# Optimization experiments

Measured on AMD Instinct MI355X. Metric: run time of the kernel, lower is better.

The kernel has to match this reference:

```python
import jax, jax.numpy as jnp
import numpy as np

N = 50000
E = 600000
C = 128          # out_channels (== in_channels)
L = 3            # num_conv layers
HID = 32
NUM_CLASSES = 7


def setup_inputs() -> dict:
    key = jax.random.key(0)
    ks = jax.random.split(key, 16)
    bound = 1.0 / np.sqrt(C)
    inp = {
        "x": jax.random.normal(ks[0], (N, C), dtype=jnp.float32),
        "edge_index": jax.random.randint(ks[1], (2, E), 0, N, dtype=jnp.int32),
        "edge_weight": jax.random.uniform(ks[2], (E,), dtype=jnp.float32),
        # GatedGraphConv weight: [num_layers, C, C], uniform(-1/sqrt(C), 1/sqrt(C))
        "conv_weight": jax.random.uniform(ks[3], (L, C, C), minval=-bound, maxval=bound, dtype=jnp.float32),
        # GRUCell params (torch layout: [3C, C] for ih and hh, gate order r,z,n)
        "w_ih": jax.random.uniform(ks[4], (3 * C, C), minval=-bound, maxval=bound, dtype=jnp.float32),
        "w_hh": jax.random.uniform(ks[5], (3 * C, C), minval=-bound, maxval=bound, dtype=jnp.float32),
        "b_ih": jax.random.uniform(ks[6], (3 * C,), minval=-bound, maxval=bound, dtype=jnp.float32),
        "b_hh": jax.random.uniform(ks[7], (3 * C,), minval=-bound, maxval=bound, dtype=jnp.float32),
        # MLP: C -> 32 -> 32 -> 32 -> NUM_CLASSES, tanh between hidden layers
        "w0": jax.random.normal(ks[8], (HID, C), dtype=jnp.float32) * 0.05,
        "b0": jnp.zeros((HID,), dtype=jnp.float32),
        "w1": jax.random.normal(ks[9], (HID, HID), dtype=jnp.float32) * 0.1,
        "b1": jnp.zeros((HID,), dtype=jnp.float32),
        "w2": jax.random.normal(ks[10], (HID, HID), dtype=jnp.float32) * 0.1,
        "b2": jnp.zeros((HID,), dtype=jnp.float32),
        "w3": jax.random.normal(ks[11], (NUM_CLASSES, HID), dtype=jnp.float32) * 0.1,
        "b3": jnp.zeros((NUM_CLASSES,), dtype=jnp.float32),
    }
    return inp


def _gru_cell(m, h, w_ih, w_hh, b_ih, b_hh):
    # torch GRUCell: gates ordered (r, z, n)
    gx = m @ w_ih.T + b_ih          # [N, 3C]
    gh = h @ w_hh.T + b_hh          # [N, 3C]
    xr, xz, xn = jnp.split(gx, 3, axis=-1)
    hr, hz, hn = jnp.split(gh, 3, axis=-1)
    r = jax.nn.sigmoid(xr + hr)
    z = jax.nn.sigmoid(xz + hz)
    n = jnp.tanh(xn + r * hn)
    return (1.0 - z) * n + z * h


def reference(x, edge_index, edge_weight, conv_weight, w_ih, w_hh, b_ih, b_hh,
              w0, b0, w1, b1, w2, b2, w3, b3):
    src, dst = edge_index[0], edge_index[1]
    h = x  # in_channels == out_channels, no padding needed
    for i in range(L):
        m = h @ conv_weight[i]                          # [N, C] dense GEMM
        msgs = edge_weight[:, None] * m[src]            # gather + edge weighting [E, C]
        agg = jax.ops.segment_sum(msgs, dst, num_segments=N)  # scatter-add [N, C]
        h = _gru_cell(agg, h, w_ih, w_hh, b_ih, b_hh)
    # MLP with tanh between hidden layers, linear last
    y = jnp.tanh(h @ w0.T + b0)
    y = jnp.tanh(y @ w1.T + b1)
    y = jnp.tanh(y @ w2.T + b2)
    y = y @ w3.T + b3
    return jax.nn.log_softmax(y, axis=-1)
```

## Files before the change

### kernel.cpp

```cpp
#include <hip/hip_runtime.h>
#include <hip/hip_bf16.h>
#include <math.h>

#define NN 50000
#define NE 600000
#define CC 128
#define NL 3
#define NRG (NN / 16)
#define C_RG 4
#define G_RG 4
#define SCAN_B 196

typedef __attribute__((ext_vector_type(8))) short bf16x8;
typedef __attribute__((ext_vector_type(4))) float f32x4;
typedef unsigned short ushort_t;
typedef unsigned int uint_t;

__device__ inline ushort_t f2bf(float f) {
    __hip_bfloat16 b = __float2bfloat16(f);
    return *reinterpret_cast<ushort_t*>(&b);
}
__device__ inline float bf2f(ushort_t u) {
    return __uint_as_float(((uint_t)u) << 16);
}
__device__ inline float fsig(float x) {
    return __builtin_amdgcn_rcpf(1.f + __builtin_amdgcn_exp2f(-1.44269504f * x));
}
__device__ inline float ftanh(float x) {
    float e = __builtin_amdgcn_exp2f(2.88539008f * fabsf(x));
    float t = 1.f - 2.f * __builtin_amdgcn_rcpf(e + 1.f);
    return copysignf(t, x);
}

__global__ __launch_bounds__(256) void k_prep(const float* __restrict__ x,
                                              ushort_t* __restrict__ h_bf,
                                              const float* __restrict__ wih,
                                              const float* __restrict__ whh,
                                              const float* __restrict__ cw,
                                              const float* __restrict__ w0,
                                              const float* __restrict__ w1,
                                              const float* __restrict__ w2,
                                              const float* __restrict__ w3,
                                              ushort_t* __restrict__ wx_pk,
                                              ushort_t* __restrict__ wh_pk,
                                              ushort_t* __restrict__ cw_pk,
                                              ushort_t* __restrict__ wm_pk,
                                              int* __restrict__ degcnt) {
    int bid = blockIdx.x;
    int t = threadIdx.x;
    if (bid < 6250) {
        size_t i = (size_t)bid * 256 + t;
        float4 v = ((const float4*)x)[i];
        ushort4 u;
        u.x = f2bf(v.x); u.y = f2bf(v.y); u.z = f2bf(v.z); u.w = f2bf(v.w);
        ((ushort4*)h_bf)[i] = u;
        return;
    }
    int bb = bid - 6250;
    if (bb < 384) {
        const float* W = (bb < 192) ? wih : whh;
        ushort_t* pk = (bb < 192) ? wx_pk : wh_pk;
        int tid = ((bb < 192) ? bb : bb - 192) * 256 + t;
        int e = tid & 7;
        int l = (tid >> 3) & 63;
        int s = (tid >> 9) & 3;
        int rest = tid >> 11;
        int g = rest % 3, c0 = rest / 3;
        int row = g * 128 + c0 * 16 + (l & 15);
        int col = s * 32 + (l >> 4) * 8 + e;
        pk[tid] = f2bf(W[row * 128 + col]);
        return;
    }
    bb -= 384;
    if (bb < 192) {
        int tid = bb * 256 + t;
        int e = tid & 7;
        int l = (tid >> 3) & 63;
        int s = (tid >> 9) & 3;
        int rest = tid >> 11;
        int c0 = rest & 7, layer = rest >> 3;
        int c = c0 * 16 + (l & 15);
        int k = s * 32 + (l >> 4) * 8 + e;
        cw_pk[tid] = f2bf(cw[layer * 16384 + k * 128 + c]);
        return;
    }
    bb -= 192;
    if (bb < 26) {
        int tid = bb * 256 + t;
        if (tid >= 6656) return;
        int e = tid & 7;
        int l = (tid >> 3) & 63;
        int lr = l & 15, lg = l >> 4;
        if (tid < 4096) {
            int s = (tid >> 9) & 3;
            int c0 = tid >> 11;
            wm_pk[tid] = f2bf(w0[(c0 * 16 + lr) * 128 + s * 32 + lg * 8 + e]);
        } else if (tid < 5120) {
            int c0 = (tid - 4096) >> 9;
            wm_pk[tid] = f2bf(w1[(c0 * 16 + lr) * 32 + lg * 8 + e]);
        } else if (tid < 6144) {
            int c0 = (tid - 5120) >> 9;
            wm_pk[tid] = f2bf(w2[(c0 * 16 + lr) * 32 + lg * 8 + e]);
        } else {
            wm_pk[tid] = (lr < 7) ? f2bf(w3[lr * 32 + lg * 8 + e]) : (ushort_t)0;
        }
        return;
    }
    bb -= 26;
    {
        int i = bb * 256 + t;
        if (i < 2 * NN) degcnt[i] = 0;
    }
}

__global__ __launch_bounds__(256) void k_count(const int* __restrict__ dst,
                                               int* __restrict__ deg) {
    int c = blockIdx.x * 256 + threadIdx.x;
    if (c >= NE / 4) return;
    int4 d4 = ((const int4*)dst)[c];
    atomicAdd(&deg[d4.x], 1);
    atomicAdd(&deg[d4.y], 1);
    atomicAdd(&deg[d4.z], 1);
    atomicAdd(&deg[d4.w], 1);
}

__global__ __launch_bounds__(256) void k_scan1(const int* __restrict__ deg,
                                               int* __restrict__ off,
                                               int* __restrict__ bsum) {
    __shared__ int sm[256];
    int t = threadIdx.x, i = blockIdx.x * 256 + t;
    int v = (i < NN) ? deg[i] : 0;
    sm[t] = v;
    __syncthreads();
#pragma unroll
    for (int ofs = 1; ofs < 256; ofs <<= 1) {
        int u = (t >= ofs) ? sm[t - ofs] : 0;
        __syncthreads();
        sm[t] += u;
        __syncthreads();
    }
    if (i < NN) off[i] = sm[t] - v;
    if (t == 255) bsum[blockIdx.x] = sm[255];
}

__global__ __launch_bounds__(256) void k_scan2(const int* __restrict__ bsum,
                                               int* __restrict__ bofs,
                                               int* __restrict__ off) {
    __shared__ int sm[256];
    int t = threadIdx.x;
    int v = (t < SCAN_B) ? bsum[t] : 0;
    sm[t] = v;
    __syncthreads();
#pragma unroll
    for (int ofs = 1; ofs < 256; ofs <<= 1) {
        int u = (t >= ofs) ? sm[t - ofs] : 0;
        __syncthreads();
        sm[t] += u;
        __syncthreads();
    }
    if (t < SCAN_B) bofs[t] = sm[t] - v;
    if (t == 255) off[NN] = sm[255];
}

__global__ __launch_bounds__(256) void k_fill(const int* __restrict__ src,
                                              const int* __restrict__ dst,
                                              const float* __restrict__ ew,
                                              const int* __restrict__ off_p,
                                              const int* __restrict__ bofs,
                                              int* __restrict__ cnt,
                                              uint2* __restrict__ e_pair) {
    int e = blockIdx.x * 256 + threadIdx.x;
    if (e >= NE) return;
    int d = dst[e];
    int p = off_p[d] + bofs[d >> 8] + atomicAdd(&cnt[d], 1);
    uint2 pr;
    pr.x = (uint_t)src[e];
    pr.y = __float_as_uint(ew[e]);
    e_pair[p] = pr;
}

__global__ __launch_bounds__(256, 2) void k_conv(const ushort_t* __restrict__ h_bf,
                                                 const ushort_t* __restrict__ cw_pk,
                                                 ushort_t* __restrict__ m_bf) {
    int wid = (blockIdx.x * 256 + threadIdx.x) >> 6;
    int l = threadIdx.x & 63;
    int lr = l & 15, lg = l >> 4;
    int c0g = wid & 3;
    int chunk = wid >> 2;

    bf16x8 B[2][4];
    {
        const bf16x8* pw = (const bf16x8*)cw_pk;
#pragma unroll
        for (int p = 0; p < 2; p++)
#pragma unroll
            for (int s = 0; s < 4; s++)
                B[p][s] = pw[(size_t)(((c0g + 4 * p) * 4 + s) * 64) + l];
    }
    int c_lo = c0g * 16 + lr;

    for (int it = 0; it < C_RG; it++) {
        int rg = chunk * C_RG + it;
        if (rg >= NRG) break;
        int n0 = rg * 16;
        const short* ap = (const short*)h_bf + (size_t)(n0 + lr) * CC + lg * 8;
        bf16x8 a[4];
#pragma unroll
        for (int s = 0; s < 4; s++) a[s] = *(const bf16x8*)(ap + s * 32);
        f32x4 acc0 = {0.f,0.f,0.f,0.f}, acc1 = {0.f,0.f,0.f,0.f};
#pragma unroll
        for (int s = 0; s < 4; s++) {
            acc0 = __builtin_amdgcn_mfma_f32_16x16x32_bf16(a[s], B[0][s], acc0, 0, 0, 0);
            acc1 = __builtin_amdgcn_mfma_f32_16x16x32_bf16(a[s], B[1][s], acc1, 0, 0, 0);
        }
#pragma unroll
        for (int j = 0; j < 4; j++) {
            size_t row = (size_t)(n0 + lg * 4 + j) * CC;
            m_bf[row + c_lo] = f2bf(acc0[j]);
            m_bf[row + c_lo + 64] = f2bf(acc1[j]);
        }
    }
}

__global__ __launch_bounds__(256) void k_agg(const int* __restrict__ off_p,
                                             const int* __restrict__ bofs,
                                             const uint2* __restrict__ e_pair,
                                             const ushort_t* __restrict__ m_bf,
                                             ushort_t* __restrict__ agg_bf) {
    int node = blockIdx.x * 4 + (threadIdx.x >> 6);
    int l = threadIdx.x & 63;
    int half = l >> 5, sl = l & 31;
    if (node >= NN) return;
    int b = off_p[node] + bofs[node >> 8];
    int e = (node == NN - 1) ? off_p[NN]
                             : off_p[node + 1] + bofs[(node + 1) >> 8];
    const uint2* m2 = (const uint2*)m_bf;
    float a0 = 0.f, a1 = 0.f, a2 = 0.f, a3 = 0.f;
    int i = b;
    for (; i + 8 <= e; i += 8) {
        uint2 p0 = e_pair[i + half];
        uint2 p1 = e_pair[i + 2 + half];
        uint2 p2 = e_pair[i + 4 + half];
        uint2 p3 = e_pair[i + 6 + half];
        uint2 v0 = m2[(size_t)p0.x * 32 + sl];
        uint2 v1 = m2[(size_t)p1.x * 32 + sl];
        uint2 v2 = m2[(size_t)p2.x * 32 + sl];
        uint2 v3 = m2[(size_t)p3.x * 32 + sl];
        float w0 = __uint_as_float(p0.y), w1 = __uint_as_float(p1.y);
        float w2 = __uint_as_float(p2.y), w3 = __uint_as_float(p3.y);
        a0 += w0 * bf2f((ushort_t)(v0.x & 0xffffu)) + w1 * bf2f((ushort_t)(v1.x & 0xffffu))
            + w2 * bf2f((ushort_t)(v2.x & 0xffffu)) + w3 * bf2f((ushort_t)(v3.x & 0xffffu));
        a1 += w0 * bf2f((ushort_t)(v0.x >> 16))     + w1 * bf2f((ushort_t)(v1.x >> 16))
            + w2 * bf2f((ushort_t)(v2.x >> 16))     + w3 * bf2f((ushort_t)(v3.x >> 16));
        a2 += w0 * bf2f((ushort_t)(v0.y & 0xffffu)) + w1 * bf2f((ushort_t)(v1.y & 0xffffu))
            + w2 * bf2f((ushort_t)(v2.y & 0xffffu)) + w3 * bf2f((ushort_t)(v3.y & 0xffffu));
        a3 += w0 * bf2f((ushort_t)(v0.y >> 16))     + w1 * bf2f((ushort_t)(v1.y >> 16))
            + w2 * bf2f((ushort_t)(v2.y >> 16))     + w3 * bf2f((ushort_t)(v3.y >> 16));
    }
    for (; i + 4 <= e; i += 4) {
        uint2 p0 = e_pair[i + half];
        uint2 p1 = e_pair[i + 2 + half];
        uint2 v0 = m2[(size_t)p0.x * 32 + sl];
        uint2 v1 = m2[(size_t)p1.x * 32 + sl];
        float w0 = __uint_as_float(p0.y), w1 = __uint_as_float(p1.y);
        a0 += w0 * bf2f((ushort_t)(v0.x & 0xffffu)) + w1 * bf2f((ushort_t)(v1.x & 0xffffu));
        a1 += w0 * bf2f((ushort_t)(v0.x >> 16))     + w1 * bf2f((ushort_t)(v1.x >> 16));
        a2 += w0 * bf2f((ushort_t)(v0.y & 0xffffu)) + w1 * bf2f((ushort_t)(v1.y & 0xffffu));
        a3 += w0 * bf2f((ushort_t)(v0.y >> 16))     + w1 * bf2f((ushort_t)(v1.y >> 16));
    }
    for (; i < e; i += 2) {
        int idx = i + half;
        uint2 pr = (idx < e) ? e_pair[idx] : make_uint2(0u, 0u);
        uint2 v = m2[(size_t)pr.x * 32 + sl];
        float w = __uint_as_float(pr.y);
        a0 += w * bf2f((ushort_t)(v.x & 0xffffu));
        a1 += w * bf2f((ushort_t)(v.x >> 16));
        a2 += w * bf2f((ushort_t)(v.y & 0xffffu));
        a3 += w * bf2f((ushort_t)(v.y >> 16));
    }
    a0 += __shfl_xor(a0, 32);
    a1 += __shfl_xor(a1, 32);
    a2 += __shfl_xor(a2, 32);
    a3 += __shfl_xor(a3, 32);
    if (half == 0) {
        uint2 p;
        p.x = (uint_t)f2bf(a0) | ((uint_t)f2bf(a1) << 16);
        p.y = (uint_t)f2bf(a2) | ((uint_t)f2bf(a3) << 16);
        ((uint2*)agg_bf)[(size_t)node * 32 + sl] = p;
    }
}

__global__ __launch_bounds__(256, 2) void k_gru(const ushort_t* __restrict__ agg_bf,
                                                const ushort_t* __restrict__ hbf_in,
                                                ushort_t* __restrict__ hbf_out,
                                                const ushort_t* __restrict__ wx_pk,
                                                const ushort_t* __restrict__ wh_pk,
                                                const float* __restrict__ b_ih,
                                                const float* __restrict__ b_hh) {
    int wid = (blockIdx.x * 256 + threadIdx.x) >> 6;
    int l = threadIdx.x & 63;
    int c0 = wid & 7;
    int chunk = wid >> 3;
    int lr = l & 15, lg = l >> 4;

    bf16x8 BX[12], BH[12];
    {
        const bf16x8* px = (const bf16x8*)wx_pk + (size_t)c0 * 12 * 64 + l;
        const bf16x8* ph = (const bf16x8*)wh_pk + (size_t)c0 * 12 * 64 + l;
#pragma unroll
        for (int f = 0; f < 12; f++) { BX[f] = px[f * 64]; BH[f] = ph[f * 64]; }
    }
    int c = c0 * 16 + lr;
    float bxr = b_ih[c], bxz = b_ih[128 + c], bxn = b_ih[256 + c];
    float bhr = b_hh[c], bhz = b_hh[128 + c], bhn = b_hh[256 + c];

    for (int it = 0; it < G_RG; it++) {
        int rg = chunk * G_RG + it;
        if (rg >= NRG) break;
        int n0 = rg * 16;
        const short* ap = (const short*)agg_bf + (size_t)(n0 + lr) * CC + lg * 8;
        const short* hp = (const short*)hbf_in + (size_t)(n0 + lr) * CC + lg * 8;
        bf16x8 a[4], hf[4];
#pragma unroll
        for (int s = 0; s < 4; s++) {
            a[s] = *(const bf16x8*)(ap + s * 32);
            hf[s] = *(const bf16x8*)(hp + s * 32);
        }
        float hv[4];
#pragma unroll
        for (int j = 0; j < 4; j++)
            hv[j] = bf2f(hbf_in[(size_t)(n0 + lg * 4 + j) * CC + c]);

        f32x4 r0 = {0.f,0.f,0.f,0.f}, r1 = {0.f,0.f,0.f,0.f}, r2 = {0.f,0.f,0.f,0.f};
        f32x4 r3 = {0.f,0.f,0.f,0.f}, r4 = {0.f,0.f,0.f,0.f}, r5 = {0.f,0.f,0.f,0.f};
#pragma unroll
        for (int s = 0; s < 4; s++) {
            r0 = __builtin_amdgcn_mfma_f32_16x16x32_bf16(a[s], BX[s], r0, 0, 0, 0);
            r1 = __builtin_amdgcn_mfma_f32_16x16x32_bf16(a[s], BX[4 + s], r1, 0, 0, 0);
            r2 = __builtin_amdgcn_mfma_f32_16x16x32_bf16(a[s], BX[8 + s], r2, 0, 0, 0);
            r3 = __builtin_amdgcn_mfma_f32_16x16x32_bf16(hf[s], BH[s], r3, 0, 0, 0);
            r4 = __builtin_amdgcn_mfma_f32_16x16x32_bf16(hf[s], BH[4 + s], r4, 0, 0, 0);
            r5 = __builtin_amdgcn_mfma_f32_16x16x32_bf16(hf[s], BH[8 + s], r5, 0, 0, 0);
        }
#pragma unroll
        for (int j = 0; j < 4; j++) {
            size_t row = (size_t)(n0 + lg * 4 + j);
            float rg_ = fsig(r0[j] + bxr + r3[j] + bhr);
            float zg = fsig(r1[j] + bxz + r4[j] + bhz);
            float ng = ftanh(r2[j] + bxn + rg_ * (r5[j] + bhn));
            float hn2 = (1.f - zg) * ng + zg * hv[j];
            hbf_out[row * CC + c] = f2bf(hn2);
        }
    }
}

__global__ __launch_bounds__(256, 2) void k_mlp(const ushort_t* __restrict__ hbf,
                                                const ushort_t* __restrict__ wm_pk,
                                                const float* __restrict__ b0,
                                                const float* __restrict__ b1,
                                                const float* __restrict__ b2,
                                                const float* __restrict__ b3,
                                                float* __restrict__ out) {
    __shared__ short vt[4][16][40];
    __shared__ float yt[4][16][8];
    int wid = (blockIdx.x * 256 + threadIdx.x) >> 6;
    int wq = threadIdx.x >> 6;
    int l = threadIdx.x & 63;
    int lr = l & 15, lg = l >> 4;

    bf16x8 W0[2][4], W1[2], W2[2], W3;
    {
        const bf16x8* pw = (const bf16x8*)wm_pk;
#pragma unroll
        for (int c0 = 0; c0 < 2; c0++)
#pragma unroll
            for (int s = 0; s < 4; s++) W0[c0][s] = pw[(c0 * 4 + s) * 64 + l];
#pragma unroll
        for (int c0 = 0; c0 < 2; c0++) {
            W1[c0] = pw[512 + c0 * 64 + l];
            W2[c0] = pw[640 + c0 * 64 + l];
        }
        W3 = pw[768 + l];
    }
    float b0v[2] = {b0[lr], b0[16 + lr]};
    float b1v[2] = {b1[lr], b1[16 + lr]};
    float b2v[2] = {b2[lr], b2[16 + lr]};
    float b3v = (lr < 7) ? b3[lr] : 0.f;

    if (wid >= NRG) return;
    int n0 = wid * 16;

    bf16x8 a[4];
    {
        const short* ap = (const short*)hbf + (size_t)(n0 + lr) * CC + lg * 8;
#pragma unroll
        for (int s = 0; s < 4; s++) a[s] = *(const bf16x8*)(ap + s * 32);
    }
#pragma unroll
    for (int c0 = 0; c0 < 2; c0++) {
        f32x4 acc = {0.f, 0.f, 0.f, 0.f};
#pragma unroll
        for (int s = 0; s < 4; s++)
            acc = __builtin_amdgcn_mfma_f32_16x16x32_bf16(a[s], W0[c0][s], acc, 0, 0, 0);
#pragma unroll
        for (int j = 0; j < 4; j++)
            vt[wq][lg * 4 + j][c0 * 16 + lr] = (short)f2bf(ftanh(acc[j] + b0v[c0]));
    }
    {
        bf16x8 av = *(const bf16x8*)&vt[wq][lr][lg * 8];
        f32x4 acc[2];
#pragma unroll
        for (int c0 = 0; c0 < 2; c0++) {
            f32x4 z = {0.f, 0.f, 0.f, 0.f};
            acc[c0] = __builtin_amdgcn_mfma_f32_16x16x32_bf16(av, W1[c0], z, 0, 0, 0);
        }
#pragma unroll
        for (int c0 = 0; c0 < 2; c0++)
#pragma unroll
            for (int j = 0; j < 4; j++)
                vt[wq][lg * 4 + j][c0 * 16 + lr] = (short)f2bf(ftanh(acc[c0][j] + b1v[c0]));
    }
    {
        bf16x8 av = *(const bf16x8*)&vt[wq][lr][lg * 8];
        f32x4 acc[2];
#pragma unroll
        for (int c0 = 0; c0 < 2; c0++) {
            f32x4 z = {0.f, 0.f, 0.f, 0.f};
            acc[c0] = __builtin_amdgcn_mfma_f32_16x16x32_bf16(av, W2[c0], z, 0, 0, 0);
        }
#pragma unroll
        for (int c0 = 0; c0 < 2; c0++)
#pragma unroll
            for (int j = 0; j < 4; j++)
                vt[wq][lg * 4 + j][c0 * 16 + lr] = (short)f2bf(ftanh(acc[c0][j] + b2v[c0]));
    }
    {
        bf16x8 av = *(const bf16x8*)&vt[wq][lr][lg * 8];
        f32x4 z = {0.f, 0.f, 0.f, 0.f};
        f32x4 acc = __builtin_amdgcn_mfma_f32_16x16x32_bf16(av, W3, z, 0, 0, 0);
        if (lr < 7) {
#pragma unroll
            for (int j = 0; j < 4; j++) yt[wq][lg * 4 + j][lr] = acc[j] + b3v;
        }
    }
    __builtin_amdgcn_s_waitcnt(0);
    if (l < 16) {
        float y[7];
#pragma unroll
        for (int j = 0; j < 7; j++) y[j] = yt[wq][l][j];
        float mx = y[0];
#pragma unroll
        for (int j = 1; j < 7; j++) mx = fmaxf(mx, y[j]);
        float se = 0.f;
#pragma unroll
        for (int j = 0; j < 7; j++) se += expf(y[j] - mx);
        float lse = mx + logf(se);
#pragma unroll
        for (int j = 0; j < 7; j++) out[(size_t)(n0 + l) * 7 + j] = y[j] - lse;
    }
}

extern "C" void kernel_launch(void* const* d_in, const int* in_sizes, int n_in,
                              void* d_out, int out_size, void* d_ws, size_t ws_size,
                              hipStream_t stream) {
    const float* x   = (const float*)d_in[0];
    const int*   ei  = (const int*)d_in[1];
    const float* ew  = (const float*)d_in[2];
    const float* cw  = (const float*)d_in[3];
    const float* wih = (const float*)d_in[4];
    const float* whh = (const float*)d_in[5];
    const float* bih = (const float*)d_in[6];
    const float* bhh = (const float*)d_in[7];
    const float* w0 = (const float*)d_in[8];
    const float* b0 = (const float*)d_in[9];
    const float* w1 = (const float*)d_in[10];
    const float* b1 = (const float*)d_in[11];
    const float* w2 = (const float*)d_in[12];
    const float* b2 = (const float*)d_in[13];
    const float* w3 = (const float*)d_in[14];
    const float* b3 = (const float*)d_in[15];
    float* out = (float*)d_out;

    ushort_t* hbf0  = (ushort_t*)d_ws;
    ushort_t* hbf1  = hbf0 + (size_t)NN * CC;
    ushort_t* m_bf  = hbf1 + (size_t)NN * CC;
    ushort_t* agg_bf= m_bf + (size_t)NN * CC;
    ushort_t* wx_pk = agg_bf + (size_t)NN * CC;
    ushort_t* wh_pk = wx_pk + 3 * CC * CC;
    ushort_t* cw_pk = wh_pk + 3 * CC * CC;
    ushort_t* wm_pk = cw_pk + 3 * CC * CC;
    uint2*    e_pair= (uint2*)(wm_pk + 6656);
    int*      off   = (int*)(e_pair + NE);
    int*      deg   = off + (NN + 1);
    int*      cnt   = deg + NN;
    int*      bsum  = cnt + NN;
    int*      bofs  = bsum + SCAN_B;

    const int* src = ei;
    const int* dst = ei + NE;

    k_prep<<<7243, 256, 0, stream>>>(x, hbf0, wih, whh, cw, w0, w1, w2, w3,
                                     wx_pk, wh_pk, cw_pk, wm_pk, deg);

    k_count<<<(NE / 4 + 255) / 256, 256, 0, stream>>>(dst, deg);
    k_scan1<<<SCAN_B, 256, 0, stream>>>(deg, off, bsum);
    k_scan2<<<1, 256, 0, stream>>>(bsum, bofs, off);
    k_fill<<<(NE + 255) / 256, 256, 0, stream>>>(src, dst, ew, off, bofs, cnt, e_pair);

    const int conv_waves = 4 * ((NRG + C_RG - 1) / C_RG);
    const int conv_blk = (conv_waves + 3) / 4;
    const int gru_waves = 8 * ((NRG + G_RG - 1) / G_RG);
    const int gru_blk = (gru_waves + 3) / 4;

    ushort_t* hin = hbf0;
    ushort_t* hout = hbf1;
    for (int l = 0; l < NL; l++) {
        k_conv<<<conv_blk, 256, 0, stream>>>(hin, cw_pk + (size_t)l * CC * CC, m_bf);
        k_agg<<<(NN + 3) / 4, 256, 0, stream>>>(off, bofs, e_pair, m_bf, agg_bf);
        k_gru<<<gru_blk, 256, 0, stream>>>(agg_bf, hin, hout, wx_pk, wh_pk, bih, bhh);
        ushort_t* tmp = hin; hin = hout; hout = tmp;
    }
    k_mlp<<<(NRG + 3) / 4, 256, 0, stream>>>(hin, wm_pk, b0, b1, b2, b3, out);
}
```

Before: 306.4 us.

## Fuse neighbor aggregation into GRU kernel via shared-memory staging

Merges the CSR gather/aggregate kernel and the GRU kernel into one kernel. Each 512-thread block aggregates 64 destination rows into an XOR-swizzled LDS tile, then eight waves each compute one 16-column slice of the GRU gates from that tile. This removes the global agg buffer write and read and one launch per layer. The trade-off is that each half-wave now handles a whole node's edges serially instead of splitting them across two halves, and the block waits at a barrier before the MFMA stage.

```diff
diff --git a/kernel.cpp b/kernel.cpp
--- a/kernel.cpp
+++ b/kernel.cpp
@@ -222,108 +222,97 @@
     }
 }
 
-__global__ __launch_bounds__(256) void k_agg(const int* __restrict__ off_p,
-                                             const int* __restrict__ bofs,
-                                             const uint2* __restrict__ e_pair,
-                                             const ushort_t* __restrict__ m_bf,
-                                             ushort_t* __restrict__ agg_bf) {
-    int node = blockIdx.x * 4 + (threadIdx.x >> 6);
-    int l = threadIdx.x & 63;
-    int half = l >> 5, sl = l & 31;
-    if (node >= NN) return;
-    int b = off_p[node] + bofs[node >> 8];
-    int e = (node == NN - 1) ? off_p[NN]
-                             : off_p[node + 1] + bofs[(node + 1) >> 8];
-    const uint2* m2 = (const uint2*)m_bf;
-    float a0 = 0.f, a1 = 0.f, a2 = 0.f, a3 = 0.f;
-    int i = b;
-    for (; i + 8 <= e; i += 8) {
-        uint2 p0 = e_pair[i + half];
-        uint2 p1 = e_pair[i + 2 + half];
-        uint2 p2 = e_pair[i + 4 + half];
-        uint2 p3 = e_pair[i + 6 + half];
-        uint2 v0 = m2[(size_t)p0.x * 32 + sl];
-        uint2 v1 = m2[(size_t)p1.x * 32 + sl];
-        uint2 v2 = m2[(size_t)p2.x * 32 + sl];
-        uint2 v3 = m2[(size_t)p3.x * 32 + sl];
-        float w0 = __uint_as_float(p0.y), w1 = __uint_as_float(p1.y);
-        float w2 = __uint_as_float(p2.y), w3 = __uint_as_float(p3.y);
-        a0 += w0 * bf2f((ushort_t)(v0.x & 0xffffu)) + w1 * bf2f((ushort_t)(v1.x & 0xffffu))
-            + w2 * bf2f((ushort_t)(v2.x & 0xffffu)) + w3 * bf2f((ushort_t)(v3.x & 0xffffu));
-        a1 += w0 * bf2f((ushort_t)(v0.x >> 16))     + w1 * bf2f((ushort_t)(v1.x >> 16))
-            + w2 * bf2f((ushort_t)(v2.x >> 16))     + w3 * bf2f((ushort_t)(v3.x >> 16));
-        a2 += w0 * bf2f((ushort_t)(v0.y & 0xffffu)) + w1 * bf2f((ushort_t)(v1.y & 0xffffu))
-            + w2 * bf2f((ushort_t)(v2.y & 0xffffu)) + w3 * bf2f((ushort_t)(v3.y & 0xffffu));
-        a3 += w0 * bf2f((ushort_t)(v0.y >> 16))     + w1 * bf2f((ushort_t)(v1.y >> 16))
-            + w2 * bf2f((ushort_t)(v2.y >> 16))     + w3 * bf2f((ushort_t)(v3.y >> 16));
-    }
-    for (; i + 4 <= e; i += 4) {
-        uint2 p0 = e_pair[i + half];
-        uint2 p1 = e_pair[i + 2 + half];
-        uint2 v0 = m2[(size_t)p0.x * 32 + sl];
-        uint2 v1 = m2[(size_t)p1.x * 32 + sl];
-        float w0 = __uint_as_float(p0.y), w1 = __uint_as_float(p1.y);
-        a0 += w0 * bf2f((ushort_t)(v0.x & 0xffffu)) + w1 * bf2f((ushort_t)(v1.x & 0xffffu));
-        a1 += w0 * bf2f((ushort_t)(v0.x >> 16))     + w1 * bf2f((ushort_t)(v1.x >> 16));
-        a2 += w0 * bf2f((ushort_t)(v0.y & 0xffffu)) + w1 * bf2f((ushort_t)(v1.y & 0xffffu));
-        a3 += w0 * bf2f((ushort_t)(v0.y >> 16))     + w1 * bf2f((ushort_t)(v1.y >> 16));
-    }
-    for (; i < e; i += 2) {
-        int idx = i + half;
-        uint2 pr = (idx < e) ? e_pair[idx] : make_uint2(0u, 0u);
-        uint2 v = m2[(size_t)pr.x * 32 + sl];
-        float w = __uint_as_float(pr.y);
-        a0 += w * bf2f((ushort_t)(v.x & 0xffffu));
-        a1 += w * bf2f((ushort_t)(v.x >> 16));
-        a2 += w * bf2f((ushort_t)(v.y & 0xffffu));
-        a3 += w * bf2f((ushort_t)(v.y >> 16));
-    }
-    a0 += __shfl_xor(a0, 32);
-    a1 += __shfl_xor(a1, 32);
-    a2 += __shfl_xor(a2, 32);
-    a3 += __shfl_xor(a3, 32);
-    if (half == 0) {
-        uint2 p;
-        p.x = (uint_t)f2bf(a0) | ((uint_t)f2bf(a1) << 16);
-        p.y = (uint_t)f2bf(a2) | ((uint_t)f2bf(a3) << 16);
-        ((uint2*)agg_bf)[(size_t)node * 32 + sl] = p;
-    }
-}
-
-__global__ __launch_bounds__(256, 2) void k_gru(const ushort_t* __restrict__ agg_bf,
-                                                const ushort_t* __restrict__ hbf_in,
-                                                ushort_t* __restrict__ hbf_out,
-                                                const ushort_t* __restrict__ wx_pk,
-                                                const ushort_t* __restrict__ wh_pk,
-                                                const float* __restrict__ b_ih,
-                                                const float* __restrict__ b_hh) {
-    int wid = (blockIdx.x * 256 + threadIdx.x) >> 6;
-    int l = threadIdx.x & 63;
-    int c0 = wid & 7;
-    int chunk = wid >> 3;
+__global__ __launch_bounds__(512, 2) void k_agru(const int* __restrict__ off_p,
+                                                 const int* __restrict__ bofs,
+                                                 const uint2* __restrict__ e_pair,
+                                                 const ushort_t* __restrict__ m_bf,
+                                                 const ushort_t* __restrict__ hbf_in,
+                                                 ushort_t* __restrict__ hbf_out,
+                                                 const ushort_t* __restrict__ wx_pk,
+                                                 const ushort_t* __restrict__ wh_pk,
+                                                 const float* __restrict__ b_ih,
+                                                 const float* __restrict__ b_hh) {
+    __shared__ uint_t agg_lds[64 * 64];
+    int t = threadIdx.x;
+    int w = t >> 6;
+    int l = t & 63;
     int lr = l & 15, lg = l >> 4;
+    int row0 = blockIdx.x * 64;
 
     bf16x8 BX[12], BH[12];
     {
-        const bf16x8* px = (const bf16x8*)wx_pk + (size_t)c0 * 12 * 64 + l;
-        const bf16x8* ph = (const bf16x8*)wh_pk + (size_t)c0 * 12 * 64 + l;
+        const bf16x8* px = (const bf16x8*)wx_pk + (size_t)w * 12 * 64 + l;
+        const bf16x8* ph = (const bf16x8*)wh_pk + (size_t)w * 12 * 64 + l;
 #pragma unroll
         for (int f = 0; f < 12; f++) { BX[f] = px[f * 64]; BH[f] = ph[f * 64]; }
     }
-    int c = c0 * 16 + lr;
+
+    {
+        int hw = t >> 5;
+        int sl = t & 31;
+        const uint2* m2 = (const uint2*)m_bf;
+#pragma unroll
+        for (int k = 0; k < 4; k++) {
+            int r = hw * 4 + k;
+            int node = row0 + r;
+            if (node < NN) {
+                int b = off_p[node] + bofs[node >> 8];
+                int e = (node == NN - 1) ? off_p[NN]
+                                         : off_p[node + 1] + bofs[(node + 1) >> 8];
+                float a0 = 0.f, a1 = 0.f, a2 = 0.f, a3 = 0.f;
+                int i = b;
+                for (; i + 4 <= e; i += 4) {
+                    uint2 p0 = e_pair[i], p1 = e_pair[i + 1];
+                    uint2 p2 = e_pair[i + 2], p3 = e_pair[i + 3];
+                    uint2 v0 = m2[(size_t)p0.x * 32 + sl];
+                    uint2 v1 = m2[(size_t)p1.x * 32 + sl];
+                    uint2 v2 = m2[(size_t)p2.x * 32 + sl];
+                    uint2 v3 = m2[(size_t)p3.x * 32 + sl];
+                    float w0 = __uint_as_float(p0.y), w1 = __uint_as_float(p1.y);
+                    float w2 = __uint_as_float(p2.y), w3 = __uint_as_float(p3.y);
+                    a0 += w0 * bf2f((ushort_t)(v0.x & 0xffffu)) + w1 * bf2f((ushort_t)(v1.x & 0xffffu))
+                        + w2 * bf2f((ushort_t)(v2.x & 0xffffu)) + w3 * bf2f((ushort_t)(v3.x & 0xffffu));
+                    a1 += w0 * bf2f((ushort_t)(v0.x >> 16))     + w1 * bf2f((ushort_t)(v1.x >> 16))
+                        + w2 * bf2f((ushort_t)(v2.x >> 16))     + w3 * bf2f((ushort_t)(v3.x >> 16));
+                    a2 += w0 * bf2f((ushort_t)(v0.y & 0xffffu)) + w1 * bf2f((ushort_t)(v1.y & 0xffffu))
+                        + w2 * bf2f((ushort_t)(v2.y & 0xffffu)) + w3 * bf2f((ushort_t)(v3.y & 0xffffu));
+                    a3 += w0 * bf2f((ushort_t)(v0.y >> 16))     + w1 * bf2f((ushort_t)(v1.y >> 16))
+                        + w2 * bf2f((ushort_t)(v2.y >> 16))     + w3 * bf2f((ushort_t)(v3.y >> 16));
+                }
+                for (; i < e; i++) {
+                    uint2 pr = e_pair[i];
+                    uint2 v = m2[(size_t)pr.x * 32 + sl];
+                    float wv = __uint_as_float(pr.y);
+                    a0 += wv * bf2f((ushort_t)(v.x & 0xffffu));
+                    a1 += wv * bf2f((ushort_t)(v.x >> 16));
+                    a2 += wv * bf2f((ushort_t)(v.y & 0xffffu));
+                    a3 += wv * bf2f((ushort_t)(v.y >> 16));
+                }
+                uint2 p;
+                p.x = (uint_t)f2bf(a0) | ((uint_t)f2bf(a1) << 16);
+                p.y = (uint_t)f2bf(a2) | ((uint_t)f2bf(a3) << 16);
+                int u = sl ^ ((r & 15) << 1);
+                *(uint2*)&agg_lds[r * 64 + u * 2] = p;
+            }
+        }
+    }
+    __syncthreads();
+
+    int c = w * 16 + lr;
     float bxr = b_ih[c], bxz = b_ih[128 + c], bxn = b_ih[256 + c];
     float bhr = b_hh[c], bhz = b_hh[128 + c], bhn = b_hh[256 + c];
 
-    for (int it = 0; it < G_RG; it++) {
-        int rg = chunk * G_RG + it;
-        if (rg >= NRG) break;
-        int n0 = rg * 16;
-        const short* ap = (const short*)agg_bf + (size_t)(n0 + lr) * CC + lg * 8;
+#pragma unroll
+    for (int rg = 0; rg < G_RG; rg++) {
+        int n0 = row0 + rg * 16;
+        if (n0 >= NN) break;
+        int rl = rg * 16 + lr;
         const short* hp = (const short*)hbf_in + (size_t)(n0 + lr) * CC + lg * 8;
         bf16x8 a[4], hf[4];
 #pragma unroll
         for (int s = 0; s < 4; s++) {
-            a[s] = *(const bf16x8*)(ap + s * 32);
+            int u = (s * 8 + lg * 2) ^ ((rl & 15) << 1);
+            a[s] = *(const bf16x8*)&agg_lds[rl * 64 + u * 2];
             hf[s] = *(const bf16x8*)(hp + s * 32);
         }
         float hv[4];
@@ -484,8 +473,7 @@
     ushort_t* hbf0  = (ushort_t*)d_ws;
     ushort_t* hbf1  = hbf0 + (size_t)NN * CC;
     ushort_t* m_bf  = hbf1 + (size_t)NN * CC;
-    ushort_t* agg_bf= m_bf + (size_t)NN * CC;
-    ushort_t* wx_pk = agg_bf + (size_t)NN * CC;
+    ushort_t* wx_pk = m_bf + (size_t)NN * CC;
     ushort_t* wh_pk = wx_pk + 3 * CC * CC;
     ushort_t* cw_pk = wh_pk + 3 * CC * CC;
     ushort_t* wm_pk = cw_pk + 3 * CC * CC;
@@ -509,15 +497,14 @@
 
     const int conv_waves = 4 * ((NRG + C_RG - 1) / C_RG);
     const int conv_blk = (conv_waves + 3) / 4;
-    const int gru_waves = 8 * ((NRG + G_RG - 1) / G_RG);
-    const int gru_blk = (gru_waves + 3) / 4;
+    const int agru_blk = (NRG + G_RG - 1) / G_RG;
 
     ushort_t* hin = hbf0;
     ushort_t* hout = hbf1;
     for (int l = 0; l < NL; l++) {
         k_conv<<<conv_blk, 256, 0, stream>>>(hin, cw_pk + (size_t)l * CC * CC, m_bf);
-        k_agg<<<(NN + 3) / 4, 256, 0, stream>>>(off, bofs, e_pair, m_bf, agg_bf);
-        k_gru<<<gru_blk, 256, 0, stream>>>(agg_bf, hin, hout, wx_pk, wh_pk, bih, bhh);
+        k_agru<<<agru_blk, 512, 0, stream>>>(off, bofs, e_pair, m_bf, hin, hout,
+                                             wx_pk, wh_pk, bih, bhh);
         ushort_t* tmp = hin; hin = hout; hout = tmp;
     }
     k_mlp<<<(NRG + 3) / 4, 256, 0, stream>>>(hin, wm_pk, b0, b1, b2, b3, out);
```

Result: slower. 411.1 us (+34.2%).

## Stage GRU gate weights in LDS shared by all waves of a block

Applied to the files above, without the earlier changes.

The GRU kernel now has each block cooperatively load its 16-column slice of the input and hidden gate weights into shared memory once. All four waves read MFMA B fragments from LDS instead of each wave holding 24 bf16x8 weight registers. The work mapping changes so every wave in a block shares the same column slice, and the launch bound is raised to 4 blocks per CU to use the freed registers for occupancy. In exchange it adds LDS reads inside the MFMA loop and a block-wide sync at kernel start.

```diff
diff --git a/kernel.cpp b/kernel.cpp
--- a/kernel.cpp
+++ b/kernel.cpp
@@ -290,32 +290,38 @@
     }
 }
 
-__global__ __launch_bounds__(256, 2) void k_gru(const ushort_t* __restrict__ agg_bf,
+__global__ __launch_bounds__(256, 4) void k_gru(const ushort_t* __restrict__ agg_bf,
                                                 const ushort_t* __restrict__ hbf_in,
                                                 ushort_t* __restrict__ hbf_out,
                                                 const ushort_t* __restrict__ wx_pk,
                                                 const ushort_t* __restrict__ wh_pk,
                                                 const float* __restrict__ b_ih,
                                                 const float* __restrict__ b_hh) {
-    int wid = (blockIdx.x * 256 + threadIdx.x) >> 6;
-    int l = threadIdx.x & 63;
-    int c0 = wid & 7;
-    int chunk = wid >> 3;
+    __shared__ ushort_t wlds[24 * 512];
+    int t = threadIdx.x;
+    int c0 = blockIdx.x & 7;
+    int chunk = blockIdx.x >> 3;
+    {
+        const uint4* sx = (const uint4*)(wx_pk + (size_t)c0 * 12 * 512);
+        const uint4* sh = (const uint4*)(wh_pk + (size_t)c0 * 12 * 512);
+        uint4* d = (uint4*)wlds;
+#pragma unroll
+        for (int i = 0; i < 3; i++) {
+            d[t + i * 256] = sx[t + i * 256];
+            d[768 + t + i * 256] = sh[t + i * 256];
+        }
+    }
+    __syncthreads();
+
+    int w = t >> 6, l = t & 63;
     int lr = l & 15, lg = l >> 4;
-
-    bf16x8 BX[12], BH[12];
-    {
-        const bf16x8* px = (const bf16x8*)wx_pk + (size_t)c0 * 12 * 64 + l;
-        const bf16x8* ph = (const bf16x8*)wh_pk + (size_t)c0 * 12 * 64 + l;
-#pragma unroll
-        for (int f = 0; f < 12; f++) { BX[f] = px[f * 64]; BH[f] = ph[f * 64]; }
-    }
     int c = c0 * 16 + lr;
     float bxr = b_ih[c], bxz = b_ih[128 + c], bxn = b_ih[256 + c];
     float bhr = b_hh[c], bhz = b_hh[128 + c], bhn = b_hh[256 + c];
+    const bf16x8* BL = (const bf16x8*)wlds;
 
     for (int it = 0; it < G_RG; it++) {
-        int rg = chunk * G_RG + it;
+        int rg = (chunk * 4 + w) * G_RG + it;
         if (rg >= NRG) break;
         int n0 = rg * 16;
         const short* ap = (const short*)agg_bf + (size_t)(n0 + lr) * CC + lg * 8;
@@ -335,12 +341,12 @@
         f32x4 r3 = {0.f,0.f,0.f,0.f}, r4 = {0.f,0.f,0.f,0.f}, r5 = {0.f,0.f,0.f,0.f};
 #pragma unroll
         for (int s = 0; s < 4; s++) {
-            r0 = __builtin_amdgcn_mfma_f32_16x16x32_bf16(a[s], BX[s], r0, 0, 0, 0);
-            r1 = __builtin_amdgcn_mfma_f32_16x16x32_bf16(a[s], BX[4 + s], r1, 0, 0, 0);
-            r2 = __builtin_amdgcn_mfma_f32_16x16x32_bf16(a[s], BX[8 + s], r2, 0, 0, 0);
-            r3 = __builtin_amdgcn_mfma_f32_16x16x32_bf16(hf[s], BH[s], r3, 0, 0, 0);
-            r4 = __builtin_amdgcn_mfma_f32_16x16x32_bf16(hf[s], BH[4 + s], r4, 0, 0, 0);
-            r5 = __builtin_amdgcn_mfma_f32_16x16x32_bf16(hf[s], BH[8 + s], r5, 0, 0, 0);
+            r0 = __builtin_amdgcn_mfma_f32_16x16x32_bf16(a[s], BL[s * 64 + l], r0, 0, 0, 0);
+            r1 = __builtin_amdgcn_mfma_f32_16x16x32_bf16(a[s], BL[(4 + s) * 64 + l], r1, 0, 0, 0);
+            r2 = __builtin_amdgcn_mfma_f32_16x16x32_bf16(a[s], BL[(8 + s) * 64 + l], r2, 0, 0, 0);
+            r3 = __builtin_amdgcn_mfma_f32_16x16x32_bf16(hf[s], BL[(12 + s) * 64 + l], r3, 0, 0, 0);
+            r4 = __builtin_amdgcn_mfma_f32_16x16x32_bf16(hf[s], BL[(16 + s) * 64 + l], r4, 0, 0, 0);
+            r5 = __builtin_amdgcn_mfma_f32_16x16x32_bf16(hf[s], BL[(20 + s) * 64 + l], r5, 0, 0, 0);
         }
 #pragma unroll
         for (int j = 0; j < 4; j++) {
@@ -509,8 +515,7 @@
 
     const int conv_waves = 4 * ((NRG + C_RG - 1) / C_RG);
     const int conv_blk = (conv_waves + 3) / 4;
-    const int gru_waves = 8 * ((NRG + G_RG - 1) / G_RG);
-    const int gru_blk = (gru_waves + 3) / 4;
+    const int gru_blk = 8 * ((NRG + 4 * G_RG - 1) / (4 * G_RG));
 
     ushort_t* hin = hbf0;
     ushort_t* hout = hbf1;
```

Measured after the change: 321.0 us. +4.8%, slower.
